# Optimization experiments

Hardware: AMD Instinct MI355X
Metric: run time of the kernel (lower is better)

## Reference

```python
import jax, jax.numpy as jnp
import numpy as np
import math

N_HEAD = 4
NORM_GROUPS = 16
EPS = 1e-5


def setup_inputs() -> dict:
    key = jax.random.key(0)
    ks = jax.random.split(key, 4)
    B, C, H, W = 2, 256, 64, 64
    return {
        "input": jax.random.normal(ks[0], (B, C, H, W), dtype=jnp.float32),
        "gn_weight": jnp.ones((C,), dtype=jnp.float32),
        "gn_bias": jnp.zeros((C,), dtype=jnp.float32),
        # 1x1 convs are plain channel matmuls: weight [out_ch, in_ch]
        "qkv_weight": jax.random.normal(ks[1], (3 * C, C), dtype=jnp.float32) / math.sqrt(C),
        "out_weight": jax.random.normal(ks[2], (C, C), dtype=jnp.float32) / math.sqrt(C),
        "out_bias": jnp.zeros((C,), dtype=jnp.float32),
    }


def _group_norm(x, weight, bias):
    B, C, H, W = x.shape
    g = x.reshape(B, NORM_GROUPS, C // NORM_GROUPS, H, W)
    mu = g.mean(axis=(2, 3, 4), keepdims=True)
    var = g.var(axis=(2, 3, 4), keepdims=True)
    g = (g - mu) * jax.lax.rsqrt(var + EPS)
    return g.reshape(B, C, H, W) * weight[:, None, None] + bias[:, None, None]


def reference(input, gn_weight, gn_bias, qkv_weight, out_weight, out_bias):
    B, C, H, W = input.shape
    head_dim = C // N_HEAD
    x = _group_norm(input, gn_weight, gn_bias)
    # 1x1 conv (no bias) -> [B, 3C, H, W] -> [B, n_head, 3*head_dim, H, W]
    qkv = jnp.einsum('bchw,oc->bohw', x, qkv_weight)
    qkv = qkv.reshape(B, N_HEAD, 3 * head_dim, H, W)
    q, k, v = jnp.split(qkv, 3, axis=2)
    # full spatial attention; note: scale is sqrt(channel), as in the source
    attn = jnp.einsum('bnchw,bncyx->bnhwyx', q, k) / math.sqrt(C)
    attn = jax.nn.softmax(attn.reshape(B, N_HEAD, H, W, H * W), axis=-1)
    attn = attn.reshape(B, N_HEAD, H, W, H, W)
    out = jnp.einsum('bnhwyx,bncyx->bnchw', attn, v).reshape(B, C, H, W)
    out = jnp.einsum('bchw,oc->bohw', out, out_weight) + out_bias[:, None, None]
    return out + input
```

## Files before the change

kernel.cpp:

```cpp
#include <hip/hip_runtime.h>

typedef __bf16        bf16x8 __attribute__((ext_vector_type(8)));
typedef float         f32x4  __attribute__((ext_vector_type(4)));
typedef unsigned short u16x4 __attribute__((ext_vector_type(4)));
typedef unsigned short u16x8 __attribute__((ext_vector_type(8)));
typedef unsigned int  u32x4  __attribute__((ext_vector_type(4)));

#define MFMA16(a,b,c) __builtin_amdgcn_mfma_f32_16x16x32_bf16((a),(b),(c),0,0,0)

static __device__ __forceinline__ unsigned short f2bf(float f) {
  unsigned int u = __builtin_bit_cast(unsigned int, f);
  u += 0x7fffu + ((u >> 16) & 1u);
  return (unsigned short)(u >> 16);
}
static __device__ __forceinline__ unsigned int pk2rne(float a, float b) {
  return (unsigned int)f2bf(a) | ((unsigned int)f2bf(b) << 16);
}
static __device__ __forceinline__ unsigned int pkrn(float a, float b) {
#if __has_builtin(__builtin_amdgcn_cvt_pk_bf16_f32)
  auto r = __builtin_amdgcn_cvt_pk_bf16_f32(a, b);
  return __builtin_bit_cast(unsigned int, r);
#else
  return pk2rne(a, b);
#endif
}
static __device__ __forceinline__ bf16x8 as_bf(u32x4 v) {
  return __builtin_bit_cast(bf16x8, v);
}
static __device__ __forceinline__ float bf2f(unsigned short u) {
  return __builtin_bit_cast(float, ((unsigned int)u) << 16);
}

#define SDIM 4096
#define CDIM 256
#define NHEAD 4
#define HDIM 64
#define NBATCH 2
#define KSPLIT 4

__global__ __launch_bounds__(256) void k_prep(const float* __restrict__ x,
                                              const float* __restrict__ wq,
                                              const float* __restrict__ wo,
                                              unsigned short* __restrict__ wqf,
                                              unsigned short* __restrict__ wof,
                                              float2* __restrict__ Sp) {
  int j = blockIdx.x, i = threadIdx.x;
  if (j < 256) {
    const float* p = x + (size_t)(j >> 3) * 65536 + (size_t)(j & 7) * 8192;
    float s = 0.f, sq = 0.f;
#pragma unroll
    for (int r = 0; r < 8; ++r) {
      float4 v = *(const float4*)(p + (r * 256 + i) * 4);
      s  += v.x + v.y + v.z + v.w;
      sq += v.x * v.x + v.y * v.y + v.z * v.z + v.w * v.w;
    }
    __shared__ float rs[256], rq[256];
    rs[i] = s; rq[i] = sq;
    __syncthreads();
    for (int off = 128; off > 0; off >>= 1) {
      if (i < off) { rs[i] += rs[i + off]; rq[i] += rq[i + off]; }
      __syncthreads();
    }
    if (i == 0) Sp[j] = make_float2(rs[0], rq[0]);
  } else {
    int t = (j - 256) * 256 + i;
#pragma unroll
    for (int u = 0; u < 2; ++u) {
      int G = t * 2 + u;
      const float* src; unsigned short* dst;
      if (G < 24576) {
        int tile = G >> 6, l = G & 63;
        src = wq + (size_t)((tile >> 3) * 16 + (l & 15)) * 256 + (tile & 7) * 32 + (l >> 4) * 8;
        dst = wqf + (size_t)G * 8;
      } else {
        int G2 = G - 24576, tile = G2 >> 6, l = G2 & 63;
        src = wo + (size_t)((tile >> 3) * 16 + (l & 15)) * 256 + (tile & 7) * 32 + (l >> 4) * 8;
        dst = wof + (size_t)G2 * 8;
      }
      float4 v0 = *(const float4*)src, v1 = *(const float4*)(src + 4);
      u16x8 r;
      r[0] = f2bf(v0.x); r[1] = f2bf(v0.y); r[2] = f2bf(v0.z); r[3] = f2bf(v0.w);
      r[4] = f2bf(v1.x); r[5] = f2bf(v1.y); r[6] = f2bf(v1.z); r[7] = f2bf(v1.w);
      *(u16x8*)dst = r;
    }
  }
}

__global__ __launch_bounds__(256) void k_gn_apply(const float* __restrict__ x,
                                                  const float2* __restrict__ Sp,
                                                  const float* __restrict__ gnw,
                                                  const float* __restrict__ gnb,
                                                  unsigned short* __restrict__ Xf) {
  __shared__ __attribute__((aligned(16))) unsigned short sT[64 * 268];
  __shared__ float2 sStat[16];
  int b = blockIdx.y, s0 = blockIdx.x * 64;
  int i = threadIdx.x, lane = i & 63, w = i >> 6;
  if (i < 16) {
    float s = 0.f, sq = 0.f;
#pragma unroll
    for (int u = 0; u < 8; ++u) {
      float2 v = Sp[(b * 16 + i) * 8 + u];
      s += v.x; sq += v.y;
    }
    float mean = s * (1.f / 65536.f);
    float var  = sq * (1.f / 65536.f) - mean * mean;
    sStat[i] = make_float2(mean, rsqrtf(var + 1e-5f));
  }
  __syncthreads();
#pragma unroll 4
  for (int r = 0; r < 64; ++r) {
    int c = r * 4 + w;
    float v = x[((size_t)(b * CDIM + c)) * SDIM + s0 + lane];
    float2 st = sStat[c >> 4];
    float nv = (v - st.x) * st.y * gnw[c] + gnb[c];
    sT[lane * 268 + c] = f2bf(nv);
  }
  __syncthreads();
  int l = i & 63, fr = i >> 6;
#pragma unroll
  for (int g = 0; g < 8; ++g) {
    int tile = fr * 8 + g, st = tile >> 3, kc = tile & 7;
    const unsigned short* src = &sT[(st * 16 + (l & 15)) * 268 + kc * 32 + (l >> 4) * 8];
    u16x4 lo = *(const u16x4*)src, hi = *(const u16x4*)(src + 4);
    unsigned short* dst = Xf + (((size_t)(b * 256 + (s0 >> 4) + st) * 8 + kc) * 64 + l) * 8;
    *(u16x4*)dst = lo;
    *(u16x4*)(dst + 4) = hi;
  }
}

__global__ __launch_bounds__(256) void k_qkv(const unsigned short* __restrict__ Wf,
                                             const unsigned short* __restrict__ Xf,
                                             unsigned short* __restrict__ Qf,
                                             unsigned short* __restrict__ Kf,
                                             unsigned short* __restrict__ Vf) {
  __shared__ __attribute__((aligned(16))) unsigned short sB[64 * 68];
  int b = blockIdx.z, s0 = blockIdx.y * 64, o0 = blockIdx.x * 64;
  int i = threadIdx.x, lane = i & 63, w = i >> 6;
  int quad = lane >> 4, m = lane & 15;
  int ot = blockIdx.x * 4 + w;
  int stg = s0 >> 4;

  f32x4 acc[4] = {};
#pragma unroll
  for (int kc = 0; kc < 8; ++kc) {
    bf16x8 aW = as_bf(*(const u32x4*)(Wf + (((size_t)ot * 8 + kc) * 64 + lane) * 8));
#pragma unroll
    for (int st = 0; st < 4; ++st) {
      bf16x8 bX = as_bf(*(const u32x4*)(Xf + ((((size_t)b * 256 + stg + st) * 8 + kc) * 64 + lane) * 8));
      acc[st] = MFMA16(aW, bX, acc[st]);
    }
  }

  int sec = (o0 >> 6) % 3;
  int h   = o0 / 192;
  int bh  = b * NHEAD + h;
  float qs = (sec == 0) ? 0.09016844f : 1.0f;
#pragma unroll
  for (int st = 0; st < 4; ++st) {
    uint2 pk = make_uint2(pk2rne(acc[st][0] * qs, acc[st][1] * qs),
                          pk2rne(acc[st][2] * qs, acc[st][3] * qs));
    *(uint2*)&sB[(st * 16 + m) * 68 + w * 16 + quad * 4] = pk;
  }
  __syncthreads();
  int lp = i & 63, qp = lp >> 4, mp = lp & 15, t = i >> 6;
  if (sec < 2) {
    unsigned short* base = (sec == 0) ? Qf : Kf;
#pragma unroll
    for (int ks = 0; ks < 2; ++ks) {
      const unsigned short* src = &sB[(t * 16 + mp) * 68 + ks * 32 + qp * 8];
      u16x4 lo = *(const u16x4*)src;
      u16x4 hi = *(const u16x4*)(src + 4);
      unsigned short* dst = base + ((((size_t)bh * 256 + (s0 >> 4) + t) * 2 + ks) * 64 + lp) * 8;
      *(u16x4*)dst = lo;
      *(u16x4*)(dst + 4) = hi;
    }
  } else {
    int kt32l = t >> 1, dts = (t & 1) * 2;
#pragma unroll
    for (int dd = 0; dd < 2; ++dd) {
      int dt = dts + dd;
      u16x8 v;
#pragma unroll
      for (int jj = 0; jj < 8; ++jj)
        v[jj] = sB[(kt32l * 32 + qp * 8 + jj) * 68 + dt * 16 + mp];
      unsigned short* dst = Vf + ((((size_t)bh * 128 + (s0 >> 5) + kt32l) * 4 + dt) * 64 + lp) * 8;
      *(u16x8*)dst = v;
    }
  }
}

template <int KS>
__global__ __launch_bounds__(256, 4) void k_attn(const unsigned short* __restrict__ Qf,
                                                 const unsigned short* __restrict__ Kf,
                                                 const unsigned short* __restrict__ Vf,
                                                 unsigned short* __restrict__ Opb,
                                                 float* __restrict__ Lp) {
  __shared__ __attribute__((aligned(16))) unsigned short smem[128 * 72];
  int bh = blockIdx.y, kk = blockIdx.z;
  int i = threadIdx.x, lane = i & 63, w = i >> 6;
  int quad = lane >> 4, m = lane & 15;
  constexpr int ITERS = SDIM / KS / 32;
  unsigned short* sP = smem + w * 1280;

  bf16x8 bq[2][2];
#pragma unroll
  for (int qt = 0; qt < 2; ++qt)
#pragma unroll
    for (int ks = 0; ks < 2; ++ks)
      bq[qt][ks] = as_bf(*(const u32x4*)(Qf +
        ((((size_t)bh * 256 + (blockIdx.x * 8 + w * 2 + qt)) * 2 + ks) * 64 + lane) * 8));

  f32x4 oacc[2][4] = {};
  float li[2] = {0.f, 0.f};

  for (int it = 0; it < ITERS; ++it) {
    bf16x8 av[4];
    int kb32 = kk * ITERS + it;
#pragma unroll
    for (int dt = 0; dt < 4; ++dt)
      av[dt] = as_bf(*(const u32x4*)(Vf +
        ((((size_t)bh * 128 + kb32) * 4 + dt) * 64 + lane) * 8));

    bf16x8 ak[2][2];
    int kb16 = kk * (ITERS * 2) + it * 2;
#pragma unroll
    for (int ky = 0; ky < 2; ++ky)
#pragma unroll
      for (int ks = 0; ks < 2; ++ks)
        ak[ky][ks] = as_bf(*(const u32x4*)(Kf +
          ((((size_t)bh * 256 + kb16 + ky) * 2 + ks) * 64 + lane) * 8));

#pragma unroll
    for (int qt = 0; qt < 2; ++qt) {
      f32x4 sc0 = {-18.f, -18.f, -18.f, -18.f};
      f32x4 sc1 = sc0;
      sc0 = MFMA16(ak[0][0], bq[qt][0], sc0);
      sc0 = MFMA16(ak[0][1], bq[qt][1], sc0);
      sc1 = MFMA16(ak[1][0], bq[qt][0], sc1);
      sc1 = MFMA16(ak[1][1], bq[qt][1], sc1);
      float p[8];
#pragma unroll
      for (int r = 0; r < 4; ++r) {
        p[r]     = __builtin_amdgcn_exp2f(sc0[r]);
        p[4 + r] = __builtin_amdgcn_exp2f(sc1[r]);
      }
      li[qt] += ((p[0] + p[1]) + (p[2] + p[3])) + ((p[4] + p[5]) + (p[6] + p[7]));
      int row = (qt * 16 + m) * 40;
      *(uint2*)&sP[row + quad * 4]      = make_uint2(pkrn(p[0], p[1]), pkrn(p[2], p[3]));
      *(uint2*)&sP[row + 16 + quad * 4] = make_uint2(pkrn(p[4], p[5]), pkrn(p[6], p[7]));
    }
#pragma unroll
    for (int qt = 0; qt < 2; ++qt) {
      bf16x8 bp = *(const bf16x8*)&sP[(qt * 16 + m) * 40 + quad * 8];
#pragma unroll
      for (int dt = 0; dt < 4; ++dt)
        oacc[qt][dt] = MFMA16(av[dt], bp, oacc[qt][dt]);
    }
  }

  size_t lg = (size_t)(kk * 8 + bh) * SDIM + blockIdx.x * 128 + w * 32;
#pragma unroll
  for (int qt = 0; qt < 2; ++qt) {
    li[qt] += __shfl_xor(li[qt], 16);
    li[qt] += __shfl_xor(li[qt], 32);
  }
  if (quad == 0) {
#pragma unroll
    for (int qt = 0; qt < 2; ++qt) Lp[lg + qt * 16 + m] = li[qt];
  }

  __syncthreads();
  unsigned short* ob = smem;
#pragma unroll
  for (int qt = 0; qt < 2; ++qt)
#pragma unroll
    for (int dt = 0; dt < 4; ++dt) {
      int ql = w * 32 + qt * 16 + m, d0 = dt * 16 + quad * 4;
      *(unsigned int*)&ob[ql * 72 + d0]     = pkrn(oacc[qt][dt][0], oacc[qt][dt][1]);
      *(unsigned int*)&ob[ql * 72 + d0 + 2] = pkrn(oacc[qt][dt][2], oacc[qt][dt][3]);
    }
  __syncthreads();
  int l = i & 63, sub = i >> 6, mp = l & 15, qp = l >> 4;
#pragma unroll
  for (int tt = 0; tt < 2; ++tt)
#pragma unroll
    for (int kc = 0; kc < 2; ++kc) {
      int t16l = sub * 2 + tt;
      u16x8 v = *(const u16x8*)&ob[(t16l * 16 + mp) * 72 + kc * 32 + qp * 8];
      size_t idx = ((((size_t)(kk * 8 + bh) * 256 + blockIdx.x * 8 + t16l) * 2 + kc) * 64 + l) * 8;
      *(u16x8*)(Opb + idx) = v;
    }
}

__global__ __launch_bounds__(256, 4) void k_proj(const unsigned short* __restrict__ Wf,
                                                 const unsigned short* __restrict__ Opb,
                                                 const float* __restrict__ Lp,
                                                 const float* __restrict__ bias,
                                                 const float* __restrict__ resid,
                                                 float* __restrict__ out) {
  __shared__ __attribute__((aligned(16))) unsigned short sPc[8 * 512];
  __shared__ float sL[4][16];
  int b = blockIdx.y, t16g = blockIdx.x, s0 = t16g * 16;
  int i = threadIdx.x, lane = i & 63, w = i >> 6;
  int quad = lane >> 4, m = lane & 15;

  if (i < 64) {
    int h = i >> 4, s = i & 15;
    float lsum = 0.f;
#pragma unroll
    for (int kk = 0; kk < KSPLIT; ++kk)
      lsum += Lp[(size_t)(kk * 8 + b * NHEAD + h) * SDIM + s0 + s];
    sL[h][s] = 1.f / lsum;
  }
  __syncthreads();

  int fr = i >> 6, l = i & 63;
#pragma unroll
  for (int f = 0; f < 2; ++f) {
    int kcq = fr * 2 + f, h = kcq >> 1, kch = kcq & 1;
    float o[8] = {};
#pragma unroll
    for (int kk = 0; kk < KSPLIT; ++kk) {
      const unsigned short* p = Opb +
        ((((size_t)(kk * 8 + b * NHEAD + h) * 256 + t16g) * 2 + kch) * 64 + l) * 8;
      u16x8 v = *(const u16x8*)p;
#pragma unroll
      for (int e = 0; e < 8; ++e) o[e] += bf2f(v[e]);
    }
    float inv = sL[h][l & 15];
    unsigned int dw[4];
#pragma unroll
    for (int e = 0; e < 4; ++e) dw[e] = pkrn(o[2 * e] * inv, o[2 * e + 1] * inv);
    *(u32x4*)&sPc[kcq * 512 + l * 8] = u32x4{dw[0], dw[1], dw[2], dw[3]};
  }
  __syncthreads();

  f32x4 acc[4] = {};
#pragma unroll
  for (int kc = 0; kc < 8; ++kc) {
    bf16x8 bP = *(const bf16x8*)&sPc[kc * 512 + lane * 8];
#pragma unroll
    for (int j = 0; j < 4; ++j) {
      int ot = w * 4 + j;
      bf16x8 aW = as_bf(*(const u32x4*)(Wf + (((size_t)ot * 8 + kc) * 64 + lane) * 8));
      acc[j] = MFMA16(aW, bP, acc[j]);
    }
  }

#pragma unroll
  for (int j = 0; j < 4; ++j)
#pragma unroll
    for (int r = 0; r < 4; ++r) {
      int o = (w * 4 + j) * 16 + quad * 4 + r;
      int s = s0 + m;
      size_t idx = ((size_t)b * CDIM + o) * SDIM + s;
      out[idx] = acc[j][r] + bias[o] + resid[idx];
    }
}

extern "C" void kernel_launch(void* const* d_in, const int* in_sizes, int n_in,
                              void* d_out, int out_size, void* d_ws, size_t ws_size,
                              hipStream_t stream) {
  const float* input = (const float*)d_in[0];
  const float* gnw   = (const float*)d_in[1];
  const float* gnb   = (const float*)d_in[2];
  const float* wq    = (const float*)d_in[3];
  const float* wo    = (const float*)d_in[4];
  const float* ob    = (const float*)d_in[5];
  float* out = (float*)d_out;

  char* ws = (char*)d_ws;
  unsigned short* Xf  = (unsigned short*)(ws);
  unsigned short* Qf  = (unsigned short*)(ws + (4ull  << 20));
  unsigned short* Kf  = (unsigned short*)(ws + (8ull  << 20));
  unsigned short* Vf  = (unsigned short*)(ws + (12ull << 20));
  unsigned short* wqf = (unsigned short*)(ws + (20ull << 20));
  unsigned short* wof = (unsigned short*)(ws + (20ull << 20) + (1u << 19));
  float2* Sp          = (float2*)(ws + (20ull << 20) + (3u << 18));
  float* Lp           = (float*)(ws + (21ull << 20));
  unsigned short* Opb = (unsigned short*)(ws + (22ull << 20));

  k_prep<<<320, 256, 0, stream>>>(input, wq, wo, wqf, wof, Sp);
  k_gn_apply<<<dim3(64, NBATCH), 256, 0, stream>>>(input, Sp, gnw, gnb, Xf);
  k_qkv<<<dim3(12, 64, NBATCH), 256, 0, stream>>>(wqf, Xf, Qf, Kf, Vf);
  k_attn<KSPLIT><<<dim3(32, NHEAD * NBATCH, KSPLIT), 256, 0, stream>>>(Qf, Kf, Vf, Opb, Lp);
  k_proj<<<dim3(256, NBATCH), 256, 0, stream>>>(wof, Opb, Lp, ob, input, out);
}
```

Measured before the change: 146.6 us.

## Keep P in registers for PV MFMA via zero-padded halves, split GN-apply by channels

The attention kernel no longer round-trips the softmax probabilities through shared memory. It builds two zero-padded bf16x8 operands directly from registers and issues two MFMAs per V tile, with the V fragment layout permuted in k_qkv to match. This removes LDS writes and reads, at the cost of doubling the PV MFMA count with half-zero operands. The GN-apply kernel is also split across 4 channel blocks, giving a smaller LDS tile and more blocks.

Result: no change. 146.6 us (-0.0%).

```diff
diff --git a/kernel.cpp b/kernel.cpp
--- a/kernel.cpp
+++ b/kernel.cpp
@@ -91,9 +91,9 @@
                                                   const float* __restrict__ gnw,
                                                   const float* __restrict__ gnb,
                                                   unsigned short* __restrict__ Xf) {
-  __shared__ __attribute__((aligned(16))) unsigned short sT[64 * 268];
+  __shared__ __attribute__((aligned(16))) unsigned short sT[64 * 68];
   __shared__ float2 sStat[16];
-  int b = blockIdx.y, s0 = blockIdx.x * 64;
+  int b = blockIdx.z, s0 = blockIdx.x * 64, c0 = blockIdx.y * 64;
   int i = threadIdx.x, lane = i & 63, w = i >> 6;
   if (i < 16) {
     float s = 0.f, sq = 0.f;
@@ -108,21 +108,21 @@
   }
   __syncthreads();
 #pragma unroll 4
-  for (int r = 0; r < 64; ++r) {
-    int c = r * 4 + w;
+  for (int r = 0; r < 16; ++r) {
+    int c = c0 + r * 4 + w;
     float v = x[((size_t)(b * CDIM + c)) * SDIM + s0 + lane];
     float2 st = sStat[c >> 4];
     float nv = (v - st.x) * st.y * gnw[c] + gnb[c];
-    sT[lane * 268 + c] = f2bf(nv);
-  }
-  __syncthreads();
-  int l = i & 63, fr = i >> 6;
-#pragma unroll
-  for (int g = 0; g < 8; ++g) {
-    int tile = fr * 8 + g, st = tile >> 3, kc = tile & 7;
-    const unsigned short* src = &sT[(st * 16 + (l & 15)) * 268 + kc * 32 + (l >> 4) * 8];
+    sT[lane * 68 + (c - c0)] = f2bf(nv);
+  }
+  __syncthreads();
+  int l = i & 63, t = i >> 6, mp = l & 15, qp = l >> 4;
+#pragma unroll
+  for (int kcl = 0; kcl < 2; ++kcl) {
+    const unsigned short* src = &sT[(t * 16 + mp) * 68 + kcl * 32 + qp * 8];
     u16x4 lo = *(const u16x4*)src, hi = *(const u16x4*)(src + 4);
-    unsigned short* dst = Xf + (((size_t)(b * 256 + (s0 >> 4) + st) * 8 + kc) * 64 + l) * 8;
+    unsigned short* dst = Xf +
+      (((size_t)(b * 256 + (s0 >> 4) + t) * 8 + (c0 >> 5) + kcl) * 64 + l) * 8;
     *(u16x4*)dst = lo;
     *(u16x4*)(dst + 4) = hi;
   }
@@ -181,8 +181,10 @@
       int dt = dts + dd;
       u16x8 v;
 #pragma unroll
-      for (int jj = 0; jj < 8; ++jj)
-        v[jj] = sB[(kt32l * 32 + qp * 8 + jj) * 68 + dt * 16 + mp];
+      for (int jj = 0; jj < 4; ++jj) {
+        v[jj]     = sB[(kt32l * 32 + qp * 4 + jj) * 68 + dt * 16 + mp];
+        v[4 + jj] = sB[(kt32l * 32 + 16 + qp * 4 + jj) * 68 + dt * 16 + mp];
+      }
       unsigned short* dst = Vf + ((((size_t)bh * 128 + (s0 >> 5) + kt32l) * 4 + dt) * 64 + lp) * 8;
       *(u16x8*)dst = v;
     }
@@ -200,7 +202,6 @@
   int i = threadIdx.x, lane = i & 63, w = i >> 6;
   int quad = lane >> 4, m = lane & 15;
   constexpr int ITERS = SDIM / KS / 32;
-  unsigned short* sP = smem + w * 1280;
 
   bf16x8 bq[2][2];
 #pragma unroll
@@ -214,12 +215,12 @@
   float li[2] = {0.f, 0.f};
 
   for (int it = 0; it < ITERS; ++it) {
-    bf16x8 av[4];
+    u32x4 vf[4];
     int kb32 = kk * ITERS + it;
 #pragma unroll
     for (int dt = 0; dt < 4; ++dt)
-      av[dt] = as_bf(*(const u32x4*)(Vf +
-        ((((size_t)bh * 128 + kb32) * 4 + dt) * 64 + lane) * 8));
+      vf[dt] = *(const u32x4*)(Vf +
+        ((((size_t)bh * 128 + kb32) * 4 + dt) * 64 + lane) * 8);
 
     bf16x8 ak[2][2];
     int kb16 = kk * (ITERS * 2) + it * 2;
@@ -245,16 +246,13 @@
         p[4 + r] = __builtin_amdgcn_exp2f(sc1[r]);
       }
       li[qt] += ((p[0] + p[1]) + (p[2] + p[3])) + ((p[4] + p[5]) + (p[6] + p[7]));
-      int row = (qt * 16 + m) * 40;
-      *(uint2*)&sP[row + quad * 4]      = make_uint2(pkrn(p[0], p[1]), pkrn(p[2], p[3]));
-      *(uint2*)&sP[row + 16 + quad * 4] = make_uint2(pkrn(p[4], p[5]), pkrn(p[6], p[7]));
-    }
-#pragma unroll
-    for (int qt = 0; qt < 2; ++qt) {
-      bf16x8 bp = *(const bf16x8*)&sP[(qt * 16 + m) * 40 + quad * 8];
-#pragma unroll
-      for (int dt = 0; dt < 4; ++dt)
-        oacc[qt][dt] = MFMA16(av[dt], bp, oacc[qt][dt]);
+      bf16x8 b0 = as_bf(u32x4{pkrn(p[0], p[1]), pkrn(p[2], p[3]), 0u, 0u});
+      bf16x8 b1 = as_bf(u32x4{0u, 0u, pkrn(p[4], p[5]), pkrn(p[6], p[7])});
+#pragma unroll
+      for (int dt = 0; dt < 4; ++dt) {
+        oacc[qt][dt] = MFMA16(as_bf(vf[dt]), b0, oacc[qt][dt]);
+        oacc[qt][dt] = MFMA16(as_bf(vf[dt]), b1, oacc[qt][dt]);
+      }
     }
   }
 
@@ -381,7 +379,7 @@
   unsigned short* Opb = (unsigned short*)(ws + (22ull << 20));
 
   k_prep<<<320, 256, 0, stream>>>(input, wq, wo, wqf, wof, Sp);
-  k_gn_apply<<<dim3(64, NBATCH), 256, 0, stream>>>(input, Sp, gnw, gnb, Xf);
+  k_gn_apply<<<dim3(64, 4, NBATCH), 256, 0, stream>>>(input, Sp, gnw, gnb, Xf);
   k_qkv<<<dim3(12, 64, NBATCH), 256, 0, stream>>>(wqf, Xf, Qf, Kf, Vf);
   k_attn<KSPLIT><<<dim3(32, NHEAD * NBATCH, KSPLIT), 256, 0, stream>>>(Qf, Kf, Vf, Opb, Lp);
   k_proj<<<dim3(256, NBATCH), 256, 0, stream>>>(wof, Opb, Lp, ob, input, out);
```
